# Kernel tuning notes

Hardware: AMD Instinct MI355X
Metric: run time of the kernel (lower is better)

The kernel has to match this reference:

```python
import jax, jax.numpy as jnp
import numpy as np

N, DIM, HEADS, E = 20000, 256, 4, 100000
C = DIM  # TransformerConv out_channels per head (concat=False averages heads)


def setup_inputs() -> dict:
    key = jax.random.key(0)
    ks = jax.random.split(key, 12)
    s = DIM ** -0.5
    w = lambda k, shape: jax.random.normal(k, shape, jnp.float32) * s
    z = lambda shape: jnp.zeros(shape, jnp.float32)
    return {
        "f_all": jax.random.normal(ks[0], (N, DIM), jnp.float32),
        "edge_index": jax.random.randint(ks[1], (2, E), 0, N),
        "W_gcn": w(ks[2], (DIM, DIM)), "b_gcn": z((DIM,)),
        "W_q": w(ks[3], (DIM, HEADS * C)), "b_q": z((HEADS * C,)),
        "W_k": w(ks[4], (DIM, HEADS * C)), "b_k": z((HEADS * C,)),
        "W_v": w(ks[5], (DIM, HEADS * C)), "b_v": z((HEADS * C,)),
        "W_skip": w(ks[6], (DIM, DIM)), "b_skip": z((DIM,)),
        "W_beta": w(ks[7], (3 * DIM, 1)),
        "W_cnn": w(ks[8], (DIM, DIM)), "b_cnn": z((DIM,)),
    }


def reference(f_all, edge_index, W_gcn, b_gcn, W_q, b_q, W_k, b_k, W_v, b_v,
              W_skip, b_skip, W_beta, W_cnn, b_cnn):
    src, dst = edge_index[0], edge_index[1]

    # --- GCNConv: add self loops, symmetric D^-1/2 (A+I) D^-1/2 normalization ---
    loop = jnp.arange(N)
    s2 = jnp.concatenate([src, loop])
    d2 = jnp.concatenate([dst, loop])
    deg = jax.ops.segment_sum(jnp.ones_like(d2, jnp.float32), d2, N)
    dinv = jnp.where(deg > 0, 1.0 / jnp.sqrt(deg), 0.0)
    norm = dinv[s2] * dinv[d2]                    # [E+N]
    h = f_all @ W_gcn                             # [N, DIM]
    x = jax.ops.segment_sum(h[s2] * norm[:, None], d2, N) + b_gcn
    x = jax.nn.relu(x)

    # --- TransformerConv(heads=H, concat=False, beta=True) ---
    q = (x @ W_q + b_q).reshape(N, HEADS, C)
    k = (x @ W_k + b_k).reshape(N, HEADS, C)
    v = (x @ W_v + b_v).reshape(N, HEADS, C)
    logits = jnp.einsum('ehc,ehc->eh', q[dst], k[src]) / np.float32(np.sqrt(C))
    m = jax.ops.segment_max(logits, dst, N)       # per-target max for stable softmax
    e = jnp.exp(logits - m[dst])
    denom = jax.ops.segment_sum(e, dst, N)
    alpha = e / jnp.maximum(denom[dst], 1e-16)    # [E, H]
    agg = jax.ops.segment_sum(v[src] * alpha[:, :, None], dst, N)  # [N, H, C]
    out = agg.mean(axis=1)                        # concat=False -> head average
    xr = x @ W_skip + b_skip                      # root/skip branch
    beta = jax.nn.sigmoid(jnp.concatenate([out, xr, out - xr], axis=-1) @ W_beta)
    tf = jax.nn.relu(beta * xr + (1.0 - beta) * out)  # [N, DIM]

    # --- Conv1d with kernel (dim,1) on [1,1,dim,N]: per-node linear, output [dim,N] ---
    conv = jnp.einsum('cd,nd->cn', W_cnn, tf) + b_cnn[:, None]  # [DIM, N]
    # torch does .view(1, n_mole, -1) on the [1,dim,1,N] conv output: raw reshape
    return conv.reshape(1, N, DIM)
```

## Files before the change

### kernel.cpp

```cpp
#include <hip/hip_runtime.h>
#include <math.h>

#define DIMC 256
#define NHEAD 4
#define CAP 64

typedef unsigned short bf16u;
typedef __attribute__((ext_vector_type(8))) short bf16x8;
typedef __attribute__((ext_vector_type(4))) float f32x4;

typedef __attribute__((address_space(1))) const unsigned char ga_u8;
typedef __attribute__((address_space(3))) unsigned char lds_u8;
__device__ __forceinline__ void gld_lds16(const void* g, void* l) {
    __builtin_amdgcn_global_load_lds((ga_u8*)g, (lds_u8*)l, 16, 0, 0);
}

__device__ __forceinline__ float bf2f(bf16u u) {
    union { float f; unsigned int i; } c; c.i = ((unsigned int)u) << 16; return c.f;
}
__device__ __forceinline__ bf16u f2bf(float f) {
    union { float f; unsigned int i; } c; c.f = f;
    unsigned int r = c.i + 0x7fffu + ((c.i >> 16) & 1u);
    return (bf16u)(r >> 16);
}
__device__ __forceinline__ void store_bf4(bf16u* p, float4 v) {
    ushort4 raw;
    raw.x = f2bf(v.x); raw.y = f2bf(v.y); raw.z = f2bf(v.z); raw.w = f2bf(v.w);
    *(ushort4*)p = raw;
}
__device__ __forceinline__ void load_bf8(const bf16u* p, float* o) {
    bf16x8 raw = *(const bf16x8*)p;
#pragma unroll
    for (int i = 0; i < 8; ++i) {
        union { float f; unsigned int u; } c;
        c.u = ((unsigned int)(unsigned short)raw[i]) << 16;
        o[i] = c.f;
    }
}
__device__ __forceinline__ void store_bf8(bf16u* p, const float* v) {
    bf16x8 raw;
#pragma unroll
    for (int i = 0; i < 8; ++i) raw[i] = (short)f2bf(v[i]);
    *(bf16x8*)p = raw;
}


__global__ void fill_kernel(const int* __restrict__ src, const int* __restrict__ dst,
                            int* __restrict__ cursor, int* __restrict__ srcs, int E) {
    int e = blockIdx.x * 256 + threadIdx.x;
    if (e < E) {
        int d = dst[e];
        int pos = atomicAdd(&cursor[d], 1);
        if (pos < CAP) srcs[d * CAP + pos] = src[e];
    }
}


__global__ __launch_bounds__(256) void prep_kernel(
    const float* __restrict__ f_all, int n4_f,
    const float* __restrict__ W_gcn, const float* __restrict__ W_q,
    const float* __restrict__ W_k, const float* __restrict__ W_v,
    const float* __restrict__ W_skip, const float* __restrict__ W_cnn,
    const float* __restrict__ b_q, const float* __restrict__ b_v,
    const float* __restrict__ b_skip,
    bf16u* __restrict__ xbuf, bf16u* __restrict__ WgcnT,
    bf16u* __restrict__ BTyp, bf16u* __restrict__ BT_vs,
    bf16u* __restrict__ Wcnn_b,
    float* __restrict__ ybias, float* __restrict__ bvm,
    int* __restrict__ cursor, int N) {
    __shared__ __align__(16) char sh[40960];
    int b = blockIdx.x, t = threadIdx.x;
    int nf = (n4_f + 255) >> 8;
    int nz = (N + 255) >> 8;

    if (b < 16) {
        bf16u (*As)[128][32] = (bf16u(*)[128][32])sh;
        bf16u (*Bs)[128][32] = (bf16u(*)[128][32])(sh + 16384);
        bf16u (*Cs)[128]     = (bf16u(*)[128])(sh + 32768);
        int rb = b >> 1, cb = b & 1;
        int h = rb >> 1;
        int j0 = (rb & 1) * 128;
        int t0 = h * 256;
        int w = t >> 6, lane = t & 63;
        int q = lane >> 4, r = lane & 15;
        int wm = (w & 1) * 64, wn = (w >> 1) * 64;
        int srow = t >> 2, scol = (t & 3) * 8;
        const float* ak0 = W_k + (size_t)(j0 + srow) * 1024 + t0 + scol;
        const float* ak1 = W_k + (size_t)(j0 + 64 + srow) * 1024 + t0 + scol;
        const float* bq0 = W_q + (size_t)(cb * 128 + srow) * 1024 + t0 + scol;
        const float* bq1 = W_q + (size_t)(cb * 128 + 64 + srow) * 1024 + t0 + scol;
        auto stage = [&](const float* gp, bf16u* lp) {
            float4 u = *(const float4*)gp, v = *(const float4*)(gp + 4);
            bf16x8 o;
            o[0] = (short)f2bf(u.x); o[1] = (short)f2bf(u.y);
            o[2] = (short)f2bf(u.z); o[3] = (short)f2bf(u.w);
            o[4] = (short)f2bf(v.x); o[5] = (short)f2bf(v.y);
            o[6] = (short)f2bf(v.z); o[7] = (short)f2bf(v.w);
            *(bf16x8*)lp = o;
        };
        f32x4 acc[4][4] = {};
        for (int g = 0; g < 4; ++g) {
            int k0 = g * 64;
            stage(ak0 + k0,      &As[0][srow][scol]);
            stage(ak1 + k0,      &As[0][64 + srow][scol]);
            stage(ak0 + k0 + 32, &As[1][srow][scol]);
            stage(ak1 + k0 + 32, &As[1][64 + srow][scol]);
            stage(bq0 + k0,      &Bs[0][srow][scol]);
            stage(bq1 + k0,      &Bs[0][64 + srow][scol]);
            stage(bq0 + k0 + 32, &Bs[1][srow][scol]);
            stage(bq1 + k0 + 32, &Bs[1][64 + srow][scol]);
            __syncthreads();
#pragma unroll
            for (int ks = 0; ks < 2; ++ks) {
                bf16x8 af[4], bfr[4];
#pragma unroll
                for (int i = 0; i < 4; ++i) af[i] = *(const bf16x8*)&As[ks][wm + i * 16 + r][q * 8];
#pragma unroll
                for (int j = 0; j < 4; ++j) bfr[j] = *(const bf16x8*)&Bs[ks][wn + j * 16 + r][q * 8];
#pragma unroll
                for (int i = 0; i < 4; ++i)
#pragma unroll
                    for (int j = 0; j < 4; ++j)
                        acc[i][j] = __builtin_amdgcn_mfma_f32_16x16x32_bf16(af[i], bfr[j], acc[i][j], 0, 0, 0);
            }
            __syncthreads();
        }
        int bm = rb * 128, bn = cb * 128;
        int rhalf = (w & 1) * 16;
        int colbase = (w >> 1) * 64;
#pragma unroll
        for (int i = 0; i < 4; ++i) {
#pragma unroll
            for (int j = 0; j < 4; ++j)
#pragma unroll
                for (int rg = 0; rg < 4; ++rg)
                    Cs[rhalf + q * 4 + rg][colbase + j * 16 + r] = f2bf(acc[i][j][rg]);
            __syncthreads();
#pragma unroll
            for (int cpass = 0; cpass < 2; ++cpass) {
                int chunk = cpass * 256 + t;
                int sr = chunk >> 4;
                int c16 = chunk & 15;
                int grow = bm + (sr < 16 ? i * 16 + sr : 64 + i * 16 + (sr - 16));
                *(bf16x8*)&BTyp[(size_t)grow * 256 + bn + c16 * 8] = *(const bf16x8*)&Cs[sr][c16 * 8];
            }
            __syncthreads();
        }
        return;
    }
    b -= 16;
    if (b < nf) {
        int i = b * 256 + t;
        if (i < n4_f) {
            float4 vv = *(const float4*)(f_all + (size_t)i * 4);
            store_bf4(xbuf + (size_t)i * 4, vv);
        }
        return;
    }
    b -= nf;
    if (b < 64) {
        int i = b * 256 + t;
        float4 vv = *(const float4*)(W_cnn + (size_t)i * 4);
        store_bf4(Wcnn_b + (size_t)i * 4, vv);
        return;
    }
    b -= 64;
    if (b < 4) {
        int h = b, j = t;
        const float4* bq4 = (const float4*)(b_q + h * 256);
        const float4* wk4 = (const float4*)(W_k + (size_t)j * 1024 + h * 256);
        float acc = 0.f;
        for (int u = 0; u < 64; ++u) {
            float4 a = bq4[u], w = wk4[u];
            acc += a.x * w.x + a.y * w.y + a.z * w.z + a.w * w.w;
        }
        ybias[h * 256 + j] = acc;
        return;
    }
    b -= 4;
    if (b < 1) {
        ybias[1024 + t] = b_skip[t];
        bvm[t] = 0.25f * (b_v[t] + b_v[256 + t] + b_v[512 + t] + b_v[768 + t]);
        return;
    }
    b -= 1;
    if (b < nz) {
        int i = b * 256 + t;
        if (i < N) cursor[i] = 0;
        return;
    }
    b -= nz;
    float (*T)[33] = (float(*)[33])sh;
    const float* src; bf16u* dst;
    int inld, inrow0, incol0, outld, outrow0, outcol0;
    if (b < 64) {
        int N0 = (b & 7) * 32, K0 = (b >> 3) * 32;
        src = W_gcn; inld = 256; inrow0 = K0; incol0 = N0;
        dst = WgcnT; outld = 256; outrow0 = N0; outcol0 = K0;
    } else if (b < 128) {
        int bb = b - 64; int N0 = (bb & 7) * 32, K0 = (bb >> 3) * 32;
        src = W_skip; inld = 256; inrow0 = K0; incol0 = N0;
        dst = BTyp;  outld = 256; outrow0 = 1024 + N0; outcol0 = K0;
    } else {
        int bb = b - 128; int jt = bb & 7, ct = (bb >> 3) & 7, hh = bb >> 6;
        src = W_v;  inld = 1024; inrow0 = ct * 32; incol0 = hh * 256 + jt * 32;
        dst = BT_vs; outld = 1024; outrow0 = jt * 32; outcol0 = hh * 256 + ct * 32;
    }
    int tx = t & 31, ty = t >> 5;
#pragma unroll
    for (int i = 0; i < 4; ++i)
        T[ty + 8 * i][tx] = src[(size_t)(inrow0 + ty + 8 * i) * inld + incol0 + tx];
    __syncthreads();
#pragma unroll
    for (int i = 0; i < 4; ++i)
        dst[(size_t)(outrow0 + ty + 8 * i) * outld + outcol0 + tx] = f2bf(T[tx][ty + 8 * i]);
}


template <bool ROWBIAS>
__global__ __launch_bounds__(256) void gemm_tile(const bf16u* __restrict__ A,
                                                 const bf16u* __restrict__ BT,
                                                 const float* __restrict__ bias,
                                                 void* __restrict__ Cout,
                                                 int M, int Nc, int ldc, int K) {
    __shared__ __align__(16) bf16u As[2][128][32];
    __shared__ __align__(16) bf16u Bs[2][128][32];
    int t = threadIdx.x;
    int w = t >> 6, lane = t & 63;
    int q = lane >> 4, r = lane & 15;
    int wm = (w & 1) * 64, wn = (w >> 1) * 64;
    int bm = blockIdx.y * 128, bn = blockIdx.x * 128;

    int srow = t >> 2, scol = (t & 3) * 8;
    int arow0 = bm + srow;      if (arow0 >= M)  arow0 = M - 1;
    int arow1 = bm + 64 + srow; if (arow1 >= M)  arow1 = M - 1;
    int brow0 = bn + srow;      if (brow0 >= Nc) brow0 = Nc - 1;
    int brow1 = bn + 64 + srow; if (brow1 >= Nc) brow1 = Nc - 1;
    const bf16u* a0 = A + (size_t)arow0 * K + scol;
    const bf16u* a1 = A + (size_t)arow1 * K + scol;
    const bf16u* b0 = BT + (size_t)brow0 * K + scol;
    const bf16u* b1 = BT + (size_t)brow1 * K + scol;

    char* As_base = (char*)&As[0][0][0] + w * 1024;
    char* Bs_base = (char*)&Bs[0][0][0] + w * 1024;

    f32x4 acc[4][4] = {};
    int ngroups = K >> 6;
    for (int g = 0; g < ngroups; ++g) {
        int k0 = g * 64;
        gld_lds16(a0 + k0, As_base);
        gld_lds16(a1 + k0, As_base + 4096);
        gld_lds16(b0 + k0, Bs_base);
        gld_lds16(b1 + k0, Bs_base + 4096);
        gld_lds16(a0 + k0 + 32, As_base + 8192);
        gld_lds16(a1 + k0 + 32, As_base + 8192 + 4096);
        gld_lds16(b0 + k0 + 32, Bs_base + 8192);
        gld_lds16(b1 + k0 + 32, Bs_base + 8192 + 4096);
        __syncthreads();
#pragma unroll
        for (int ks = 0; ks < 2; ++ks) {
            bf16x8 af[4], bfr[4];
#pragma unroll
            for (int i = 0; i < 4; ++i) af[i] = *(const bf16x8*)&As[ks][wm + i * 16 + r][q * 8];
#pragma unroll
            for (int j = 0; j < 4; ++j) bfr[j] = *(const bf16x8*)&Bs[ks][wn + j * 16 + r][q * 8];
#pragma unroll
            for (int i = 0; i < 4; ++i)
#pragma unroll
                for (int j = 0; j < 4; ++j)
                    acc[i][j] = __builtin_amdgcn_mfma_f32_16x16x32_bf16(af[i], bfr[j], acc[i][j], 0, 0, 0);
        }
        __syncthreads();
    }

    if (ROWBIAS) {
        float* C = (float*)Cout;
#pragma unroll
        for (int j = 0; j < 4; ++j) {
            int col = bn + wn + j * 16 + r;
            if (col >= Nc) continue;
#pragma unroll
            for (int i = 0; i < 4; ++i)
#pragma unroll
                for (int rg = 0; rg < 4; ++rg) {
                    int row = bm + wm + i * 16 + q * 4 + rg;
                    if (row < M)
                        __builtin_nontemporal_store(acc[i][j][rg] + bias[row],
                                                    &C[(size_t)row * ldc + col]);
                }
        }
    } else {
        __shared__ __align__(16) bf16u Cs[32][128];
        bf16u* C = (bf16u*)Cout;
        float cb4[4];
#pragma unroll
        for (int j = 0; j < 4; ++j) {
            int col = bn + wn + j * 16 + r;
            cb4[j] = bias ? bias[col] : 0.0f;
        }
        int rhalf = (w & 1) * 16;
        int colbase = (w >> 1) * 64;
        __syncthreads();
#pragma unroll
        for (int i = 0; i < 4; ++i) {
#pragma unroll
            for (int j = 0; j < 4; ++j)
#pragma unroll
                for (int rg = 0; rg < 4; ++rg)
                    Cs[rhalf + q * 4 + rg][colbase + j * 16 + r] = f2bf(acc[i][j][rg] + cb4[j]);
            __syncthreads();
#pragma unroll
            for (int cpass = 0; cpass < 2; ++cpass) {
                int chunk = cpass * 256 + t;
                int sr = chunk >> 4;
                int c16 = chunk & 15;
                int grow = bm + (sr < 16 ? i * 16 + sr : 64 + i * 16 + (sr - 16));
                if (grow < M)
                    __builtin_nontemporal_store(*(const bf16x8*)&Cs[sr][c16 * 8],
                                                (bf16x8*)&C[(size_t)grow * ldc + bn + c16 * 8]);
            }
            __syncthreads();
        }
    }
}


__global__ __launch_bounds__(256) void gcn_agg_kernel(const bf16u* __restrict__ h,
                                                      const int* __restrict__ cursor,
                                                      const int* __restrict__ srcs,
                                                      const float* __restrict__ b_gcn,
                                                      bf16u* __restrict__ x, int N) {
    int n = blockIdx.x * 8 + (threadIdx.x >> 5);
    if (n >= N) return;
    int lane = threadIdx.x & 31;
    int cb = lane * 8;
    int cnt = cursor[n]; if (cnt > CAP) cnt = CAP;
    float dn = rsqrtf((float)(cnt + 1));
    float hn[8];
    load_bf8(h + (size_t)n * DIMC + cb, hn);
    int base = n * CAP;
    float acc[8] = {};
    int iters = (cnt + 3) >> 2;
    for (int it = 0; it < iters; ++it) {
        int e0 = it * 4, nv = cnt - e0;
        int i0, i1, i2, i3;
        if (nv >= 4) {
            int4 s4 = *(const int4*)(srcs + base + e0);
            i0 = s4.x; i1 = s4.y; i2 = s4.z; i3 = s4.w;
        } else {
            i0 = srcs[base + e0];
            i1 = srcs[base + (nv > 1 ? e0 + 1 : e0)];
            i2 = srcs[base + (nv > 2 ? e0 + 2 : e0)];
            i3 = i2;
        }
        float d0 = rsqrtf((float)(cursor[i0] + 1));
        float d1 = nv > 1 ? rsqrtf((float)(cursor[i1] + 1)) : 0.f;
        float d2 = nv > 2 ? rsqrtf((float)(cursor[i2] + 1)) : 0.f;
        float d3 = nv > 3 ? rsqrtf((float)(cursor[i3] + 1)) : 0.f;
        float h0[8], h1[8], h2[8], h3[8];
        load_bf8(h + (size_t)i0 * DIMC + cb, h0);
        load_bf8(h + (size_t)i1 * DIMC + cb, h1);
        load_bf8(h + (size_t)i2 * DIMC + cb, h2);
        load_bf8(h + (size_t)i3 * DIMC + cb, h3);
#pragma unroll
        for (int j = 0; j < 8; ++j)
            acc[j] += (h0[j] * d0 + h1[j] * d1) + (h2[j] * d2 + h3[j] * d3);
    }
    float4 bg0 = *(const float4*)(b_gcn + cb);
    float4 bg1 = *(const float4*)(b_gcn + cb + 4);
    float bg[8] = {bg0.x, bg0.y, bg0.z, bg0.w, bg1.x, bg1.y, bg1.z, bg1.w};
    float dnn = dn * dn;
    float o[8];
#pragma unroll
    for (int j = 0; j < 8; ++j) o[j] = fmaxf(dn * acc[j] + hn[j] * dnn + bg[j], 0.f);
    store_bf8(x + (size_t)n * DIMC + cb, o);
}


__global__ __launch_bounds__(256) void attn_kernel(const bf16u* __restrict__ Y, int ldy,
                                                   const bf16u* __restrict__ x,
                                                   const int* __restrict__ cursor,
                                                   const int* __restrict__ srcs,
                                                   bf16u* __restrict__ Z, int N) {
    int n = blockIdx.x * 4 + (threadIdx.x >> 6);
    if (n >= N) return;
    int lane = threadIdx.x & 63;
    int hq = lane >> 4;
    int r = lane & 15;
    const float scale = 0.0625f;

    float yv[16];
    const bf16u* yrow = Y + (size_t)n * ldy + hq * DIMC + r * 16;
    load_bf8(yrow, yv);
    load_bf8(yrow + 8, yv + 8);
#pragma unroll
    for (int j = 0; j < 16; ++j) yv[j] *= scale;

    int cnt = cursor[n]; if (cnt > CAP) cnt = CAP;
    int base = n * CAP;
    float m = -INFINITY, denom = 0.f;
    float acc[16];
#pragma unroll
    for (int j = 0; j < 16; ++j) acc[j] = 0.f;

    int iters = (cnt + 3) >> 2;
    for (int it = 0; it < iters; ++it) {
        int e0 = it * 4, nv = cnt - e0;
        int i0, i1, i2, i3;
        if (nv >= 4) {
            int4 s4 = *(const int4*)(srcs + base + e0);
            i0 = s4.x; i1 = s4.y; i2 = s4.z; i3 = s4.w;
        } else {
            i0 = srcs[base + e0];
            i1 = srcs[base + (nv > 1 ? e0 + 1 : e0)];
            i2 = srcs[base + (nv > 2 ? e0 + 2 : e0)];
            i3 = i2;
        }
        const bf16u* p0 = x + (size_t)i0 * DIMC + r * 16;
        const bf16u* p1 = x + (size_t)i1 * DIMC + r * 16;
        const bf16u* p2 = x + (size_t)i2 * DIMC + r * 16;
        const bf16u* p3 = x + (size_t)i3 * DIMC + r * 16;
        float x0[16], x1[16], x2[16], x3[16];
        load_bf8(p0, x0); load_bf8(p0 + 8, x0 + 8);
        load_bf8(p1, x1); load_bf8(p1 + 8, x1 + 8);
        load_bf8(p2, x2); load_bf8(p2 + 8, x2 + 8);
        load_bf8(p3, x3); load_bf8(p3 + 8, x3 + 8);
        float d0 = 0.f, d1 = 0.f, d2 = 0.f, d3 = 0.f;
#pragma unroll
        for (int j = 0; j < 16; ++j) {
            d0 += yv[j] * x0[j]; d1 += yv[j] * x1[j];
            d2 += yv[j] * x2[j]; d3 += yv[j] * x3[j];
        }
#pragma unroll
        for (int msk = 1; msk <= 8; msk <<= 1) {
            d0 += __shfl_xor(d0, msk, 64); d1 += __shfl_xor(d1, msk, 64);
            d2 += __shfl_xor(d2, msk, 64); d3 += __shfl_xor(d3, msk, 64);
        }
        if (nv < 2) d1 = -INFINITY;
        if (nv < 3) d2 = -INFINITY;
        if (nv < 4) d3 = -INFINITY;
        float mx = fmaxf(fmaxf(d0, d1), fmaxf(d2, d3));
        float nm = fmaxf(m, mx);
        float so = __expf(m - nm);
        float e0p = __expf(d0 - nm), e1p = __expf(d1 - nm);
        float e2p = __expf(d2 - nm), e3p = __expf(d3 - nm);
        denom = denom * so + (e0p + e1p) + (e2p + e3p);
#pragma unroll
        for (int j = 0; j < 16; ++j)
            acc[j] = acc[j] * so + (e0p * x0[j] + e1p * x1[j]) + (e2p * x2[j] + e3p * x3[j]);
        m = nm;
    }

    float inv = 0.25f / fmaxf(denom, 1e-16f);
    float o[16];
#pragma unroll
    for (int j = 0; j < 16; ++j) o[j] = acc[j] * inv;
    bf16u* zrow = Z + (size_t)n * 1024 + hq * DIMC + r * 16;
    store_bf8(zrow, o);
    store_bf8(zrow + 8, o + 8);
}


__global__ __launch_bounds__(256) void beta_kernel(const bf16u* __restrict__ outz,
                                                   const bf16u* __restrict__ Yp, int ldy,
                                                   const float* __restrict__ bvm,
                                                   const float* __restrict__ W_beta,
                                                   const int* __restrict__ cursor,
                                                   bf16u* __restrict__ tf, int N) {
    int n = blockIdx.x * 8 + (threadIdx.x >> 5);
    if (n >= N) return;
    int lane = threadIdx.x & 31;
    int cb = lane * 8;
    float ov[8], xr[8];
    load_bf8(outz + (size_t)n * DIMC + cb, ov);
    load_bf8(Yp + (size_t)n * ldy + 1024 + cb, xr);
    float gate = (cursor[n] > 0) ? 1.f : 0.f;
#pragma unroll
    for (int j = 0; j < 8; ++j) ov[j] += gate * bvm[cb + j];
    float contrib = 0.f;
#pragma unroll
    for (int j = 0; j < 8; ++j) {
        float w1 = W_beta[cb + j];
        float w2 = W_beta[256 + cb + j];
        float w3 = W_beta[512 + cb + j];
        contrib += ov[j] * w1 + xr[j] * w2 + (ov[j] - xr[j]) * w3;
    }
#pragma unroll
    for (int msk = 1; msk <= 16; msk <<= 1) contrib += __shfl_xor(contrib, msk, 64);
    float beta = 1.0f / (1.0f + __expf(-contrib));
    float tv[8];
#pragma unroll
    for (int j = 0; j < 8; ++j) tv[j] = fmaxf(beta * xr[j] + (1.0f - beta) * ov[j], 0.f);
    store_bf8(tf + (size_t)n * DIMC + cb, tv);
}


static inline size_t align_up(size_t x) { return (x + 255) & ~(size_t)255; }

extern "C" void kernel_launch(void* const* d_in, const int* in_sizes, int n_in,
                              void* d_out, int out_size, void* d_ws, size_t ws_size,
                              hipStream_t stream) {
    const float* f_all  = (const float*)d_in[0];
    const int*   eidx   = (const int*)d_in[1];
    const float* W_gcn  = (const float*)d_in[2];
    const float* b_gcn  = (const float*)d_in[3];
    const float* W_q    = (const float*)d_in[4];
    const float* b_q    = (const float*)d_in[5];
    const float* W_k    = (const float*)d_in[6];
    const float* W_v    = (const float*)d_in[8];
    const float* b_v    = (const float*)d_in[9];
    const float* W_skip = (const float*)d_in[10];
    const float* b_skip = (const float*)d_in[11];
    const float* W_beta = (const float*)d_in[12];
    const float* W_cnn  = (const float*)d_in[13];
    const float* b_cnn  = (const float*)d_in[14];

    const int N = in_sizes[0] / DIMC;
    const int E = in_sizes[1] / 2;
    const int* src = eidx;
    const int* dst = eidx + E;

    char* p = (char*)d_ws;
    auto alloc = [&](size_t bytes) { char* r = p; p += align_up(bytes); return r; };
    int*   cursor = (int*)alloc((size_t)N * 4);
    int*   srcs   = (int*)alloc((size_t)N * CAP * 4);
    bf16u* WgcnT  = (bf16u*)alloc(256 * 256 * 2);
    bf16u* BTyp   = (bf16u*)alloc((size_t)1280 * 256 * 2);
    bf16u* BT_vs  = (bf16u*)alloc((size_t)256 * 1024 * 2);
    bf16u* Wcnn_b = (bf16u*)alloc(256 * 256 * 2);
    float* ybias  = (float*)alloc(1280 * 4);
    float* bvm    = (float*)alloc(256 * 4);
    bf16u* xbuf   = (bf16u*)alloc((size_t)N * DIMC * 2);
    bf16u* h      = (bf16u*)alloc((size_t)N * DIMC * 2);
    bf16u* Yp     = (bf16u*)alloc((size_t)N * 1280 * 2);
    bf16u* Z      = (bf16u*)alloc((size_t)N * 1024 * 2);
    bf16u* outz   = (bf16u*)alloc((size_t)N * DIMC * 2);

    int n4_f = N * DIMC / 4;
    int nf = (n4_f + 255) >> 8;
    int nz = (N + 255) >> 8;
    prep_kernel<<<16 + nf + 64 + 4 + 1 + nz + 384, 256, 0, stream>>>(
        f_all, n4_f, W_gcn, W_q, W_k, W_v, W_skip, W_cnn,
        b_q, b_v, b_skip, xbuf, WgcnT, BTyp, BT_vs, Wcnn_b,
        ybias, bvm, cursor, N);

    fill_kernel<<<(E + 255) / 256, 256, 0, stream>>>(src, dst, cursor, srcs, E);

    int mby = (N + 127) / 128;
    gemm_tile<false><<<dim3(2, mby), 256, 0, stream>>>(xbuf, WgcnT, nullptr, h, N, 256, 256, 256);
    gcn_agg_kernel<<<(N + 7) / 8, 256, 0, stream>>>(h, cursor, srcs, b_gcn, xbuf, N);
    gemm_tile<false><<<dim3(10, mby), 256, 0, stream>>>(xbuf, BTyp, ybias, Yp, N, 1280, 1280, 256);
    attn_kernel<<<(N + 3) / 4, 256, 0, stream>>>(Yp, 1280, xbuf, cursor, srcs, Z, N);
    gemm_tile<false><<<dim3(2, mby), 256, 0, stream>>>(Z, BT_vs, nullptr, outz, N, 256, 256, 1024);
    beta_kernel<<<(N + 7) / 8, 256, 0, stream>>>(outz, Yp, 1280, bvm, W_beta, cursor, h, N);
    gemm_tile<true><<<dim3((N + 127) / 128, 2), 256, 0, stream>>>(
        Wcnn_b, h, b_cnn, (float*)d_out, 256, N, N, 256);
}
```

Measured before the change: 262.3 us.

## Stage neighbor rows through LDS with prefetch in attention; simplify GCN tail loop

The attention kernel used to have each of the four head groups load the same neighbor x rows straight from global memory. It now loads each row once, cooperatively across the wave, into a per-wave LDS slot, two edges per iteration, and prefetches the next pair into registers while the current pair is computed. This cuts redundant global gathers and overlaps load latency with compute, at the cost of half the edge batching and reliance on an lgkmcnt wait with no explicit barrier. The GCN aggregation loop is also split into a 4-wide main loop and a scalar tail, which removes predicated dummy loads.

New measurement: 254.3 us. 3.0% less time.

```diff
diff --git a/kernel.cpp b/kernel.cpp
--- a/kernel.cpp
+++ b/kernel.cpp
@@ -15,9 +15,6 @@
     __builtin_amdgcn_global_load_lds((ga_u8*)g, (lds_u8*)l, 16, 0, 0);
 }
 
-__device__ __forceinline__ float bf2f(bf16u u) {
-    union { float f; unsigned int i; } c; c.i = ((unsigned int)u) << 16; return c.f;
-}
 __device__ __forceinline__ bf16u f2bf(float f) {
     union { float f; unsigned int i; } c; c.f = f;
     unsigned int r = c.i + 0x7fffu + ((c.i >> 16) & 1u);
@@ -340,31 +337,29 @@
     load_bf8(h + (size_t)n * DIMC + cb, hn);
     int base = n * CAP;
     float acc[8] = {};
-    int iters = (cnt + 3) >> 2;
-    for (int it = 0; it < iters; ++it) {
-        int e0 = it * 4, nv = cnt - e0;
-        int i0, i1, i2, i3;
-        if (nv >= 4) {
-            int4 s4 = *(const int4*)(srcs + base + e0);
-            i0 = s4.x; i1 = s4.y; i2 = s4.z; i3 = s4.w;
-        } else {
-            i0 = srcs[base + e0];
-            i1 = srcs[base + (nv > 1 ? e0 + 1 : e0)];
-            i2 = srcs[base + (nv > 2 ? e0 + 2 : e0)];
-            i3 = i2;
-        }
-        float d0 = rsqrtf((float)(cursor[i0] + 1));
-        float d1 = nv > 1 ? rsqrtf((float)(cursor[i1] + 1)) : 0.f;
-        float d2 = nv > 2 ? rsqrtf((float)(cursor[i2] + 1)) : 0.f;
-        float d3 = nv > 3 ? rsqrtf((float)(cursor[i3] + 1)) : 0.f;
+    int i = 0;
+    for (; i + 4 <= cnt; i += 4) {
+        int4 s4 = *(const int4*)(srcs + base + i);
+        float d0 = rsqrtf((float)(cursor[s4.x] + 1));
+        float d1 = rsqrtf((float)(cursor[s4.y] + 1));
+        float d2 = rsqrtf((float)(cursor[s4.z] + 1));
+        float d3 = rsqrtf((float)(cursor[s4.w] + 1));
         float h0[8], h1[8], h2[8], h3[8];
-        load_bf8(h + (size_t)i0 * DIMC + cb, h0);
-        load_bf8(h + (size_t)i1 * DIMC + cb, h1);
-        load_bf8(h + (size_t)i2 * DIMC + cb, h2);
-        load_bf8(h + (size_t)i3 * DIMC + cb, h3);
+        load_bf8(h + (size_t)s4.x * DIMC + cb, h0);
+        load_bf8(h + (size_t)s4.y * DIMC + cb, h1);
+        load_bf8(h + (size_t)s4.z * DIMC + cb, h2);
+        load_bf8(h + (size_t)s4.w * DIMC + cb, h3);
 #pragma unroll
         for (int j = 0; j < 8; ++j)
-            acc[j] += (h0[j] * d0 + h1[j] * d1) + (h2[j] * d2 + h3[j] * d3);
+            acc[j] += h0[j] * d0 + h1[j] * d1 + h2[j] * d2 + h3[j] * d3;
+    }
+    for (; i < cnt; ++i) {
+        int s = srcs[base + i];
+        float ds = rsqrtf((float)(cursor[s] + 1));
+        float hv[8];
+        load_bf8(h + (size_t)s * DIMC + cb, hv);
+#pragma unroll
+        for (int j = 0; j < 8; ++j) acc[j] += hv[j] * ds;
     }
     float4 bg0 = *(const float4*)(b_gcn + cb);
     float4 bg1 = *(const float4*)(b_gcn + cb + 4);
@@ -382,7 +377,9 @@
                                                    const int* __restrict__ cursor,
                                                    const int* __restrict__ srcs,
                                                    bf16u* __restrict__ Z, int N) {
-    int n = blockIdx.x * 4 + (threadIdx.x >> 6);
+    __shared__ __align__(16) bf16u xs[4][2][256];
+    int wv = threadIdx.x >> 6;
+    int n = blockIdx.x * 4 + wv;
     if (n >= N) return;
     int lane = threadIdx.x & 63;
     int hq = lane >> 4;
@@ -403,52 +400,58 @@
 #pragma unroll
     for (int j = 0; j < 16; ++j) acc[j] = 0.f;
 
-    int iters = (cnt + 3) >> 2;
+    int rl = lane >> 5;
+    int rc = (lane & 31) * 8;
+    bf16u* myslot = &xs[wv][rl][rc];
+
+    int iters = (cnt + 1) >> 1;
+    int i0 = 0, i1 = 0;
+    if (cnt > 1) {
+        int2 ss = *(const int2*)(srcs + base);
+        i0 = ss.x; i1 = ss.y;
+    } else if (cnt == 1) {
+        i0 = srcs[base]; i1 = i0;
+    }
+    bf16x8 raw;
+    if (iters > 0)
+        raw = *(const bf16x8*)(x + (size_t)(rl ? i1 : i0) * DIMC + rc);
+
     for (int it = 0; it < iters; ++it) {
-        int e0 = it * 4, nv = cnt - e0;
-        int i0, i1, i2, i3;
-        if (nv >= 4) {
-            int4 s4 = *(const int4*)(srcs + base + e0);
-            i0 = s4.x; i1 = s4.y; i2 = s4.z; i3 = s4.w;
-        } else {
-            i0 = srcs[base + e0];
-            i1 = srcs[base + (nv > 1 ? e0 + 1 : e0)];
-            i2 = srcs[base + (nv > 2 ? e0 + 2 : e0)];
-            i3 = i2;
-        }
-        const bf16u* p0 = x + (size_t)i0 * DIMC + r * 16;
-        const bf16u* p1 = x + (size_t)i1 * DIMC + r * 16;
-        const bf16u* p2 = x + (size_t)i2 * DIMC + r * 16;
-        const bf16u* p3 = x + (size_t)i3 * DIMC + r * 16;
-        float x0[16], x1[16], x2[16], x3[16];
-        load_bf8(p0, x0); load_bf8(p0 + 8, x0 + 8);
-        load_bf8(p1, x1); load_bf8(p1 + 8, x1 + 8);
-        load_bf8(p2, x2); load_bf8(p2 + 8, x2 + 8);
-        load_bf8(p3, x3); load_bf8(p3 + 8, x3 + 8);
-        float d0 = 0.f, d1 = 0.f, d2 = 0.f, d3 = 0.f;
-#pragma unroll
-        for (int j = 0; j < 16; ++j) {
-            d0 += yv[j] * x0[j]; d1 += yv[j] * x1[j];
-            d2 += yv[j] * x2[j]; d3 += yv[j] * x3[j];
-        }
+        *(bf16x8*)myslot = raw;
+        int e2 = (it + 1) * 2;
+        int nv2 = cnt - e2;
+        if (nv2 > 1) {
+            int2 ss = *(const int2*)(srcs + base + e2);
+            i0 = ss.x; i1 = ss.y;
+        } else if (nv2 == 1) {
+            i0 = srcs[base + e2]; i1 = i0;
+        }
+        if (nv2 > 0)
+            raw = *(const bf16x8*)(x + (size_t)(rl ? i1 : i0) * DIMC + rc);
+        asm volatile("s_waitcnt lgkmcnt(0)" ::: "memory");
+        float x0[16], x1[16];
+        load_bf8(&xs[wv][0][r * 16], x0);
+        load_bf8(&xs[wv][0][r * 16 + 8], x0 + 8);
+        load_bf8(&xs[wv][1][r * 16], x1);
+        load_bf8(&xs[wv][1][r * 16 + 8], x1 + 8);
+        float d0 = 0.f, d1 = 0.f;
+#pragma unroll
+        for (int j = 0; j < 16; ++j) { d0 += yv[j] * x0[j]; d1 += yv[j] * x1[j]; }
 #pragma unroll
         for (int msk = 1; msk <= 8; msk <<= 1) {
-            d0 += __shfl_xor(d0, msk, 64); d1 += __shfl_xor(d1, msk, 64);
-            d2 += __shfl_xor(d2, msk, 64); d3 += __shfl_xor(d3, msk, 64);
-        }
-        if (nv < 2) d1 = -INFINITY;
-        if (nv < 3) d2 = -INFINITY;
-        if (nv < 4) d3 = -INFINITY;
-        float mx = fmaxf(fmaxf(d0, d1), fmaxf(d2, d3));
-        float nm = fmaxf(m, mx);
+            d0 += __shfl_xor(d0, msk, 64);
+            d1 += __shfl_xor(d1, msk, 64);
+        }
+        if ((cnt & 1) && it == iters - 1) d1 = -INFINITY;
+        float nm = fmaxf(m, fmaxf(d0, d1));
         float so = __expf(m - nm);
-        float e0p = __expf(d0 - nm), e1p = __expf(d1 - nm);
-        float e2p = __expf(d2 - nm), e3p = __expf(d3 - nm);
-        denom = denom * so + (e0p + e1p) + (e2p + e3p);
-#pragma unroll
-        for (int j = 0; j < 16; ++j)
-            acc[j] = acc[j] * so + (e0p * x0[j] + e1p * x1[j]) + (e2p * x2[j] + e3p * x3[j]);
+        float p0 = __expf(d0 - nm);
+        float p1 = __expf(d1 - nm);
+        denom = denom * so + p0 + p1;
+#pragma unroll
+        for (int j = 0; j < 16; ++j) acc[j] = acc[j] * so + p0 * x0[j] + p1 * x1[j];
         m = nm;
+        asm volatile("" ::: "memory");
     }
 
     float inv = 0.25f / fmaxf(denom, 1e-16f);
```
